# Optimization experiments

Hardware: AMD Instinct MI355X
Metric: run time of the kernel (lower is better)

## Reference

```python
import jax, jax.numpy as jnp
import numpy as np

D_MODEL = 768
N_HEADS = 12
NUM_EXPERTS = 4
TOP_K = 2
SPAN_LEN = 64
GATE_HIDDEN = 128


def setup_inputs() -> dict:
    key = jax.random.key(0)
    ks = jax.random.split(key, 14)
    B, T, C, E = 4, 4096, D_MODEL, NUM_EXPERTS
    s = 0.02
    return {
        "hidden_states": jax.random.normal(ks[0], (B, T, C), jnp.float32),
        "Wq": jax.random.normal(ks[1], (E, C, C), jnp.float32) * s,
        "bq": jnp.zeros((E, C), jnp.float32),
        "Wk": jax.random.normal(ks[2], (E, C, C), jnp.float32) * s,
        "bk": jnp.zeros((E, C), jnp.float32),
        "Wv": jax.random.normal(ks[3], (E, C, C), jnp.float32) * s,
        "bv": jnp.zeros((E, C), jnp.float32),
        "gW1": jax.random.normal(ks[4], (GATE_HIDDEN, C), jnp.float32) * s,
        "gb1": jnp.zeros((GATE_HIDDEN,), jnp.float32),
        "gW2": jax.random.normal(ks[5], (E, GATE_HIDDEN), jnp.float32) * s,
        "gb2": jnp.zeros((E,), jnp.float32),
        "Wo": jax.random.normal(ks[6], (C, C), jnp.float32) * s,
        "bo": jnp.zeros((C,), jnp.float32),
    }


def _moe_proj(w, x, W, b):
    # per-expert projection then gate-weighted sum over experts
    # x: (B,N,S,C), W: (E,O,C), w: (B,N,E)
    proj = jnp.einsum("bnsc,eoc->ebnso", x, W)          # (E,B,N,S,C)
    out = jnp.einsum("bne,ebnso->bnso", w, proj)
    out = out + jnp.einsum("bne,eo->bno", w, b)[:, :, None, :]
    return out


def reference(hidden_states, Wq, bq, Wk, bk, Wv, bv, gW1, gb1, gW2, gb2, Wo, bo):
    B, T, C = hidden_states.shape
    S, H, E, K = SPAN_LEN, N_HEADS, NUM_EXPERTS, TOP_K
    Dh = C // H
    N = T // S  # T is a multiple of span_len -> no padding, all-ones masks
    x = hidden_states.reshape(B, N, S, C)

    # gating: mean-pool per span -> MLP -> top-k softmax scattered to E slots
    pooled = x.mean(axis=2)                                  # (B,N,C)
    h = jax.nn.relu(pooled @ gW1.T + gb1)
    logits = h @ gW2.T + gb2                                 # (B,N,E)
    vals, idx = jax.lax.top_k(logits, K)
    sm = jax.nn.softmax(vals, axis=-1)                       # (B,N,K)
    w = jnp.sum(jax.nn.one_hot(idx, E, dtype=sm.dtype) * sm[..., None], axis=-2)  # (B,N,E)
    entropy = -jnp.mean(jnp.sum(w * jnp.log(jnp.clip(w, 1e-9)), axis=-1))

    # gate-weighted expert QKV projections
    q = _moe_proj(w, x, Wq, bq).reshape(B, N, S, H, Dh)
    k = _moe_proj(w, x, Wk, bk).reshape(B, N, S, H, Dh)
    v = _moe_proj(w, x, Wv, bv).reshape(B, N, S, H, Dh)

    # per-span attention (mask is all ones; dropout in eval mode)
    scores = jnp.einsum("bnshd,bnthd->bnhst", q, k) / jnp.sqrt(jnp.float32(Dh))
    attn = jax.nn.softmax(scores, axis=-1)
    out = jnp.einsum("bnhst,bnthd->bnshd", attn, v).reshape(B, T, C)
    out = out @ Wo.T + bo
    return out, entropy
```

## Files before the change

kernel.cpp:

```cpp
#include <hip/hip_runtime.h>
#include <hip/hip_bf16.h>
#include <hip/hip_fp16.h>

typedef _Float16 f16;
typedef _Float16 f16x8 __attribute__((ext_vector_type(8)));
typedef _Float16 f16x4 __attribute__((ext_vector_type(4)));
typedef float f32x4 __attribute__((ext_vector_type(4)));

constexpr int B = 4;
constexpr int T = 4096;
constexpr int C = 768;
constexpr int NH = 12;
constexpr int DH = 64;
constexpr int E = 4;
constexpr int SPAN = 64;
constexpr int N = T / SPAN;
constexpr int BN = B * N;
constexpr int GH = 128;
constexpr int BTC = B * T * C;

constexpr int U_WO = C * C / 8;

#define LGKM_BARRIER()                                      \
    do {                                                    \
        asm volatile("s_waitcnt lgkmcnt(0)" ::: "memory");  \
        __builtin_amdgcn_s_barrier();                       \
        __builtin_amdgcn_sched_barrier(0);                  \
    } while (0)

__global__ __launch_bounds__(768) void cvt_x_pool(
    const float* __restrict__ x, f16* __restrict__ x16,
    float* __restrict__ pooled) {
    int span = blockIdx.x;
    int tid = threadIdx.x;
    int u = tid % 96, rg = tid / 96;
    __shared__ f16x8 xlds[6144];
    __shared__ float part[8][C];

    const float* xb = x + (size_t)span * SPAN * C;
    float a8[8] = {};
    #pragma unroll
    for (int j = 0; j < 8; ++j) {
        int r = rg * 8 + j;
        const float4* s = (const float4*)(xb + (size_t)r * C + u * 8);
        float4 A = s[0], Bv = s[1];
        f16x8 o;
        o[0] = (f16)A.x;  o[1] = (f16)A.y;  o[2] = (f16)A.z;  o[3] = (f16)A.w;
        o[4] = (f16)Bv.x; o[5] = (f16)Bv.y; o[6] = (f16)Bv.z; o[7] = (f16)Bv.w;
        xlds[r * 96 + (u & ~7) + ((u & 7) ^ (r & 7))] = o;
        a8[0] += A.x;  a8[1] += A.y;  a8[2] += A.z;  a8[3] += A.w;
        a8[4] += Bv.x; a8[5] += Bv.y; a8[6] += Bv.z; a8[7] += Bv.w;
    }
    #pragma unroll
    for (int j = 0; j < 8; ++j) part[rg][u * 8 + j] = a8[j];
    __syncthreads();
    float s = 0.f;
    #pragma unroll
    for (int g = 0; g < 8; ++g) s += part[g][tid];
    pooled[(size_t)span * C + tid] = s * (1.f / 64.f);

    f16x8* xo = (f16x8*)x16 + (size_t)span * 6144;
    #pragma unroll
    for (int j = 0; j < 8; ++j) {
        int un = tid + j * 768;
        int lr = un & 15, lg = (un >> 4) & 3, m = (un >> 6) & 3, kt = un >> 8;
        int row = m * 16 + lr, ku = kt * 4 + lg;
        xo[un] = xlds[row * 96 + (ku & ~7) + ((ku & 7) ^ (row & 7))];
    }
}

__global__ __launch_bounds__(768) void cvt_w_frag(
    const float* __restrict__ Wq, const float* __restrict__ Wk,
    const float* __restrict__ Wv,
    f16* __restrict__ Wq16, f16* __restrict__ Wk16, f16* __restrict__ Wv16) {
    int slice = blockIdx.x;
    int tsel  = blockIdx.y;
    const float* src; f16* dst;
    if (tsel == 0)      { src = Wq; dst = Wq16; }
    else if (tsel == 1) { src = Wk; dst = Wk16; }
    else                { src = Wv; dst = Wv16; }
    int e = slice / 12, cb = slice % 12;

    __shared__ f16x8 wlds[6144];
    int tid = threadIdx.x;

    const float* wb = src + ((size_t)e * C + cb * 64) * C;
    #pragma unroll
    for (int j = 0; j < 8; ++j) {
        int g = tid + j * 768;
        int row = g / 96, ku = g % 96;
        const float4* sp = (const float4*)(wb + (size_t)row * C + ku * 8);
        float4 A = sp[0], Bv = sp[1];
        f16x8 o;
        o[0] = (f16)A.x;  o[1] = (f16)A.y;  o[2] = (f16)A.z;  o[3] = (f16)A.w;
        o[4] = (f16)Bv.x; o[5] = (f16)Bv.y; o[6] = (f16)Bv.z; o[7] = (f16)Bv.w;
        wlds[row * 96 + (ku & ~7) + ((ku & 7) ^ (row & 7))] = o;
    }
    __syncthreads();

    f16x8* wo = (f16x8*)dst + (size_t)slice * 6144;
    #pragma unroll
    for (int j = 0; j < 8; ++j) {
        int un = tid + j * 768;
        int lr = un & 15, lg = (un >> 4) & 3, nn = (un >> 6) & 3, kt = un >> 8;
        int row = nn * 16 + lr, ku = kt * 4 + lg;
        wo[un] = wlds[row * 96 + (ku & ~7) + ((ku & 7) ^ (row & 7))];
    }
}

__global__ void cvt_wo(const float* __restrict__ Wo, f16* __restrict__ Wo16) {
    int i = blockIdx.x * blockDim.x + threadIdx.x;
    int stride = gridDim.x * blockDim.x;
    for (; i < U_WO; i += stride) {
        float4 a = ((const float4*)Wo)[2 * i];
        float4 b = ((const float4*)Wo)[2 * i + 1];
        f16x8 o;
        o[0] = (f16)a.x; o[1] = (f16)a.y; o[2] = (f16)a.z; o[3] = (f16)a.w;
        o[4] = (f16)b.x; o[5] = (f16)b.y; o[6] = (f16)b.z; o[7] = (f16)b.w;
        ((f16x8*)Wo16)[i] = o;
    }
}

__global__ __launch_bounds__(128) void gate_mlp(
    const float* __restrict__ pooled,
    const float* __restrict__ gW1, const float* __restrict__ gb1,
    const float* __restrict__ gW2, const float* __restrict__ gb2,
    int* __restrict__ eidx, float* __restrict__ ewts,
    float* __restrict__ ent_partial) {
    int span = blockIdx.x;
    int tid = threadIdx.x;
    __shared__ float pl[C];
    __shared__ float h[GH];
    __shared__ float logits[E];

    for (int c = tid; c < C; c += 128) pl[c] = pooled[(size_t)span * C + c];
    __syncthreads();

    {
        float acc = gb1[tid];
        const float* wrow = gW1 + (size_t)tid * C;
        #pragma unroll 8
        for (int c = 0; c < C; ++c) acc += pl[c] * wrow[c];
        h[tid] = acc > 0.f ? acc : 0.f;
    }
    __syncthreads();

    if (tid < E) {
        float acc = gb2[tid];
        const float* wrow = gW2 + (size_t)tid * GH;
        #pragma unroll 8
        for (int j = 0; j < GH; ++j) acc += h[j] * wrow[j];
        logits[tid] = acc;
    }
    __syncthreads();

    if (tid == 0) {
        int i0 = 0; float v0 = logits[0];
        for (int e = 1; e < E; ++e) { if (logits[e] > v0) { v0 = logits[e]; i0 = e; } }
        int i1 = -1; float v1 = -3.0e38f;
        for (int e = 0; e < E; ++e) { if (e != i0 && logits[e] > v1) { v1 = logits[e]; i1 = e; } }
        float bq_ = expf(v1 - v0);
        float s = 1.f + bq_;
        float sm0 = 1.f / s;
        float sm1 = bq_ / s;
        eidx[span * 2 + 0] = i0;
        eidx[span * 2 + 1] = i1;
        ewts[span * 2 + 0] = sm0;
        ewts[span * 2 + 1] = sm1;
        float p0 = fmaxf(sm0, 1e-9f), p1 = fmaxf(sm1, 1e-9f);
        ent_partial[span] = sm0 * logf(p0) + sm1 * logf(p1);
    }
}

__global__ void entropy_kernel(const float* __restrict__ ent_partial, float* __restrict__ out_ent) {
    __shared__ float sh[256];
    int tid = threadIdx.x;
    sh[tid] = ent_partial[tid];
    __syncthreads();
    for (int s = 128; s > 0; s >>= 1) {
        if (tid < s) sh[tid] += sh[tid + s];
        __syncthreads();
    }
    if (tid == 0) *out_ent = -sh[0] * (1.0f / (float)BN);
}

__global__ __launch_bounds__(256, 2) void qkv_mfma(
    const f16* __restrict__ xh,
    const f16* __restrict__ Wq16, const float* __restrict__ bq,
    const f16* __restrict__ Wk16, const float* __restrict__ bk,
    const f16* __restrict__ Wv16, const float* __restrict__ bv,
    const int* __restrict__ eidx, const float* __restrict__ ewts,
    f16* __restrict__ q16, f16* __restrict__ k16, f16* __restrict__ vt)
{
    int span  = blockIdx.x;
    int otile = blockIdx.y;
    int proj  = blockIdx.z;

    const f16* W; const float* bias; f16* out;
    if (proj == 0)      { W = Wq16; bias = bq; out = q16; }
    else if (proj == 1) { W = Wk16; bias = bk; out = k16; }
    else                { W = Wv16; bias = bv; out = vt; }

    int e0 = eidx[span * 2 + 0], e1 = eidx[span * 2 + 1];
    float w0 = ewts[span * 2 + 0], w1 = ewts[span * 2 + 1];
    f16 w0h = (f16)w0, w1h = (f16)w1;

    int tid = threadIdx.x;
    int lane = tid & 63, wv = tid >> 6;
    int lr = lane & 15, lg = lane >> 4;
    int cb = otile * 4 + wv;

    const f16x8* xu  = (const f16x8*)xh + (size_t)span * 6144 + lane;
    const f16x8* wu0 = (const f16x8*)W + ((size_t)e0 * 12 + cb) * 6144 + lane;
    const f16x8* wu1 = (const f16x8*)W + ((size_t)e1 * 12 + cb) * 6144 + lane;

    f32x4 acc[4][4] = {};

    f16x8 bb0[3][4], bb1[3][4];
    f16x8 aa[2][4];

    #pragma unroll
    for (int n = 0; n < 4; ++n) { bb0[0][n] = wu0[n * 64];        bb1[0][n] = wu1[n * 64]; }
    #pragma unroll
    for (int n = 0; n < 4; ++n) { bb0[1][n] = wu0[(4 + n) * 64];  bb1[1][n] = wu1[(4 + n) * 64]; }
    #pragma unroll
    for (int m = 0; m < 4; ++m) aa[0][m] = xu[m * 64];

    #pragma unroll
    for (int kt = 0; kt < 24; ++kt) {
        if (kt < 22) {
            int kn = kt + 2, s = (kt + 2) % 3;
            #pragma unroll
            for (int n = 0; n < 4; ++n) {
                bb0[s][n] = wu0[(kn * 4 + n) * 64];
                bb1[s][n] = wu1[(kn * 4 + n) * 64];
            }
        }
        if (kt < 23) {
            int kn = kt + 1, s = (kt + 1) & 1;
            #pragma unroll
            for (int m = 0; m < 4; ++m) aa[s][m] = xu[(kn * 4 + m) * 64];
        }

        {
            int s3 = kt % 3, s2 = kt & 1;
            __builtin_amdgcn_s_setprio(1);
            #pragma unroll
            for (int n = 0; n < 4; ++n) {
                f16x8 bf = bb0[s3][n] * w0h + bb1[s3][n] * w1h;
                #pragma unroll
                for (int m = 0; m < 4; ++m)
                    acc[m][n] = __builtin_amdgcn_mfma_f32_16x16x32_f16(aa[s2][m], bf, acc[m][n], 0, 0, 0);
            }
            __builtin_amdgcn_s_setprio(0);
        }
    }

    if (proj == 2) {
        f16* vtb = out + (size_t)span * C * 64;
        #pragma unroll
        for (int n = 0; n < 4; ++n) {
            int col = cb * 64 + n * 16 + lr;
            float be = w0 * bias[(size_t)e0 * C + col] + w1 * bias[(size_t)e1 * C + col];
            #pragma unroll
            for (int m = 0; m < 4; ++m) {
                f16x4 pk;
                #pragma unroll
                for (int r = 0; r < 4; ++r) pk[r] = (f16)(acc[m][n][r] + be);
                *(f16x4*)&vtb[(size_t)col * 64 + m * 16 + lg * 4] = pk;
            }
        }
    } else {
        f16* outb = out + (size_t)span * 64 * C;
        #pragma unroll
        for (int n = 0; n < 4; ++n) {
            int col = cb * 64 + n * 16 + lr;
            float be = w0 * bias[(size_t)e0 * C + col] + w1 * bias[(size_t)e1 * C + col];
            #pragma unroll
            for (int m = 0; m < 4; ++m) {
                #pragma unroll
                for (int r = 0; r < 4; ++r) {
                    int row = m * 16 + lg * 4 + r;
                    outb[(size_t)row * C + col] = (f16)(acc[m][n][r] + be);
                }
            }
        }
    }
}

__global__ __launch_bounds__(256) void attn_mfma(
    const f16* __restrict__ q16, const f16* __restrict__ k16,
    const f16* __restrict__ vt, f16* __restrict__ a16)
{
    int h = blockIdx.x, span = blockIdx.y;
    __shared__ __align__(16) f16 Klds[64 * 72];
    __shared__ __align__(16) f16 Vlds[64 * 72];
    __shared__ __align__(16) f16 Plds[64 * 72];

    int tid = threadIdx.x;
    int lane = tid & 63, mt = tid >> 6;
    int lr = lane & 15, lg = lane >> 4;

    const f16x8* ku = (const f16x8*)k16;
    const f16x8* vu = (const f16x8*)vt;
    #pragma unroll
    for (int i = 0; i < 2; ++i) {
        int id = tid + i * 256;
        int r = id >> 3, u = id & 7;
        *(f16x8*)&Klds[r * 72 + u * 8] = ku[(size_t)span * 6144 + (size_t)r * 96 + h * 8 + u];
        *(f16x8*)&Vlds[r * 72 + u * 8] = vu[(size_t)span * 6144 + (size_t)(h * 64 + r) * 8 + u];
    }
    const f16x8* qu = (const f16x8*)q16;
    f16x8 qa[2];
    #pragma unroll
    for (int kk = 0; kk < 2; ++kk)
        qa[kk] = qu[(size_t)span * 6144 + (size_t)(mt * 16 + lr) * 96 + h * 8 + kk * 4 + lg];

    LGKM_BARRIER();

    f32x4 accs[4] = {};
    #pragma unroll
    for (int nt = 0; nt < 4; ++nt) {
        #pragma unroll
        for (int kk = 0; kk < 2; ++kk) {
            f16x8 kb = *(const f16x8*)&Klds[(nt * 16 + lr) * 72 + kk * 32 + lg * 8];
            accs[nt] = __builtin_amdgcn_mfma_f32_16x16x32_f16(qa[kk], kb, accs[nt], 0, 0, 0);
        }
    }

    #pragma unroll
    for (int nt = 0; nt < 4; ++nt) accs[nt] *= 0.125f;
    f32x4 m4;
    #pragma unroll
    for (int r = 0; r < 4; ++r)
        m4[r] = fmaxf(fmaxf(accs[0][r], accs[1][r]), fmaxf(accs[2][r], accs[3][r]));
    #pragma unroll
    for (int st = 1; st < 16; st <<= 1) {
        #pragma unroll
        for (int r = 0; r < 4; ++r) m4[r] = fmaxf(m4[r], __shfl_xor(m4[r], st));
    }
    f32x4 ps[4];
    f32x4 sum4 = {0.f, 0.f, 0.f, 0.f};
    #pragma unroll
    for (int nt = 0; nt < 4; ++nt)
        #pragma unroll
        for (int r = 0; r < 4; ++r) {
            ps[nt][r] = __expf(accs[nt][r] - m4[r]);
            sum4[r] += ps[nt][r];
        }
    #pragma unroll
    for (int st = 1; st < 16; st <<= 1) {
        #pragma unroll
        for (int r = 0; r < 4; ++r) sum4[r] += __shfl_xor(sum4[r], st);
    }
    f32x4 inv4;
    #pragma unroll
    for (int r = 0; r < 4; ++r) inv4[r] = 1.0f / sum4[r];

    #pragma unroll
    for (int nt = 0; nt < 4; ++nt)
        #pragma unroll
        for (int r = 0; r < 4; ++r)
            Plds[(mt * 16 + lg * 4 + r) * 72 + nt * 16 + lr] = (f16)ps[nt][r];

    LGKM_BARRIER();

    f16x8 pa[2];
    #pragma unroll
    for (int kkt = 0; kkt < 2; ++kkt)
        pa[kkt] = *(const f16x8*)&Plds[(mt * 16 + lr) * 72 + kkt * 32 + lg * 8];
    f32x4 acco[4] = {};
    #pragma unroll
    for (int nt = 0; nt < 4; ++nt) {
        #pragma unroll
        for (int kkt = 0; kkt < 2; ++kkt) {
            f16x8 vb = *(const f16x8*)&Vlds[(nt * 16 + lr) * 72 + kkt * 32 + lg * 8];
            acco[nt] = __builtin_amdgcn_mfma_f32_16x16x32_f16(pa[kkt], vb, acco[nt], 0, 0, 0);
        }
    }

    #pragma unroll
    for (int nt = 0; nt < 4; ++nt)
        #pragma unroll
        for (int r = 0; r < 4; ++r)
            Klds[(mt * 16 + lg * 4 + r) * 72 + nt * 16 + lr] = (f16)(acco[nt][r] * inv4[r]);

    LGKM_BARRIER();

    int row = mt * 16 + (lane >> 2);
    int u2 = (lane & 3) * 2;
    f16x8 o0 = *(const f16x8*)&Klds[row * 72 + u2 * 8];
    f16x8 o1 = *(const f16x8*)&Klds[row * 72 + u2 * 8 + 8];
    f16x8* au = (f16x8*)a16;
    au[(size_t)span * 6144 + (size_t)row * 96 + h * 8 + u2]     = o0;
    au[(size_t)span * 6144 + (size_t)row * 96 + h * 8 + u2 + 1] = o1;
}

__global__ __launch_bounds__(512) void outproj_mfma(
    const f16* __restrict__ ah, const f16* __restrict__ Wo16,
    const float* __restrict__ bo, float* __restrict__ Y)
{
    int rt = blockIdx.x;
    int otile = blockIdx.y;

    __shared__ f16x8 as_u[128 * 8];
    __shared__ f16x8 ws_u[256 * 8];

    const f16x8* au  = (const f16x8*)(ah + (size_t)rt * 128 * C);
    const f16x8* Wou = (const f16x8*)(Wo16 + (size_t)otile * 256 * C);

    int tid = threadIdx.x;
    int lane = tid & 63, wv = tid >> 6;
    int lr = lane & 15, lg = lane >> 4;
    int wm = (wv >> 2) * 64;
    int wn = (wv & 3) * 64;

    f32x4 acc[4][4] = {};

    f16x8 ar_[2], wr_[4];
    #pragma unroll
    for (int i = 0; i < 2; ++i) {
        int id = tid + i * 512;
        ar_[i] = au[(size_t)(id >> 3) * 96 + (id & 7)];
    }
    #pragma unroll
    for (int i = 0; i < 4; ++i) {
        int id = tid + i * 512;
        wr_[i] = Wou[(size_t)(id >> 3) * 96 + (id & 7)];
    }

    for (int kc8 = 0; kc8 < 96; kc8 += 8) {
        #pragma unroll
        for (int i = 0; i < 2; ++i) {
            int id = tid + i * 512;
            int r = id >> 3, u = id & 7;
            as_u[r * 8 + (u ^ (r & 7))] = ar_[i];
        }
        #pragma unroll
        for (int i = 0; i < 4; ++i) {
            int id = tid + i * 512;
            int r = id >> 3, u = id & 7;
            ws_u[r * 8 + (u ^ (r & 7))] = wr_[i];
        }

        if (kc8 < 88) {
            int kn = kc8 + 8;
            #pragma unroll
            for (int i = 0; i < 2; ++i) {
                int id = tid + i * 512;
                ar_[i] = au[(size_t)(id >> 3) * 96 + kn + (id & 7)];
            }
            #pragma unroll
            for (int i = 0; i < 4; ++i) {
                int id = tid + i * 512;
                wr_[i] = Wou[(size_t)(id >> 3) * 96 + kn + (id & 7)];
            }
        }

        LGKM_BARRIER();

        #pragma unroll
        for (int kk = 0; kk < 2; ++kk) {
            int ub = kk * 4 + lg;
            f16x8 afrag[4], bfrag[4];
            #pragma unroll
            for (int m = 0; m < 4; ++m) {
                int r = wm + m * 16 + lr;
                afrag[m] = as_u[r * 8 + (ub ^ (r & 7))];
            }
            #pragma unroll
            for (int n = 0; n < 4; ++n) {
                int r = wn + n * 16 + lr;
                bfrag[n] = ws_u[r * 8 + (ub ^ (r & 7))];
            }
            #pragma unroll
            for (int m = 0; m < 4; ++m)
                #pragma unroll
                for (int n = 0; n < 4; ++n)
                    acc[m][n] = __builtin_amdgcn_mfma_f32_16x16x32_f16(afrag[m], bfrag[n], acc[m][n], 0, 0, 0);
        }

        LGKM_BARRIER();
    }

    #pragma unroll
    for (int n = 0; n < 4; ++n) {
        int col = otile * 256 + wn + n * 16 + lr;
        float be = bo[col];
        #pragma unroll
        for (int m = 0; m < 4; ++m) {
            #pragma unroll
            for (int r = 0; r < 4; ++r) {
                int row = rt * 128 + wm + m * 16 + lg * 4 + r;
                Y[(size_t)row * C + col] = acc[m][n][r] + be;
            }
        }
    }
}

extern "C" void kernel_launch(void* const* d_in, const int* in_sizes, int n_in,
                              void* d_out, int out_size, void* d_ws, size_t ws_size,
                              hipStream_t stream) {
    const float* x   = (const float*)d_in[0];
    const float* Wq  = (const float*)d_in[1];
    const float* bq  = (const float*)d_in[2];
    const float* Wk  = (const float*)d_in[3];
    const float* bk  = (const float*)d_in[4];
    const float* Wv  = (const float*)d_in[5];
    const float* bv  = (const float*)d_in[6];
    const float* gW1 = (const float*)d_in[7];
    const float* gb1 = (const float*)d_in[8];
    const float* gW2 = (const float*)d_in[9];
    const float* gb2 = (const float*)d_in[10];
    const float* Wo  = (const float*)d_in[11];
    const float* bo  = (const float*)d_in[12];

    float* out = (float*)d_out;

    char* ws = (char*)d_ws;
    const size_t h_btc = (size_t)BTC * sizeof(f16);
    f16* x16  = (f16*)(ws);
    f16* q16  = (f16*)(ws + 1 * h_btc);
    f16* k16  = (f16*)(ws + 2 * h_btc);
    f16* vt16 = (f16*)(ws + 3 * h_btc);
    f16* a16  = (f16*)(ws + 4 * h_btc);
    size_t off = 5 * h_btc;
    const size_t wsz = (size_t)E * C * C * sizeof(f16);
    f16* Wq16 = (f16*)(ws + off); off += wsz;
    f16* Wk16 = (f16*)(ws + off); off += wsz;
    f16* Wv16 = (f16*)(ws + off); off += wsz;
    f16* Wo16 = (f16*)(ws + off); off += (size_t)C * C * sizeof(f16);
    int*   eidx = (int*)(ws + off); off += 2048;
    float* ewts = (float*)(ws + off); off += 2048;
    float* entp = (float*)(ws + off); off += 1024;
    float* pooled = (float*)(ws + off); off += (size_t)BN * C * sizeof(float);

    cvt_x_pool<<<dim3(BN), dim3(768), 0, stream>>>(x, x16, pooled);
    cvt_w_frag<<<dim3(48, 3), dim3(768), 0, stream>>>(Wq, Wk, Wv,
                                                      Wq16, Wk16, Wv16);
    cvt_wo<<<dim3(288), dim3(256), 0, stream>>>(Wo, Wo16);
    gate_mlp<<<dim3(BN), dim3(128), 0, stream>>>(pooled, gW1, gb1, gW2, gb2,
                                                 eidx, ewts, entp);
    entropy_kernel<<<dim3(1), dim3(256), 0, stream>>>(entp, out + BTC);

    qkv_mfma<<<dim3(BN, 3, 3), dim3(256), 0, stream>>>(x16, Wq16, bq, Wk16, bk, Wv16, bv,
                                                       eidx, ewts, q16, k16, vt16);
    attn_mfma<<<dim3(NH, BN), dim3(256), 0, stream>>>(q16, k16, vt16, a16);
    outproj_mfma<<<dim3(128, 3), dim3(512), 0, stream>>>(a16, Wo16, bo, out);
}
```

Baseline: 209.5 us.

## Pair spans sharing the same expert pair to reuse weight loads in QKV GEMM

Adds a small kernel that groups spans by their unordered top-2 expert pair and packs them two per slot. The QKV kernel then processes two spans per block with a halved output-column tile, so each weight fragment loaded from global memory serves both spans. This halves per-span weight traffic. In exchange it adds a serial single-block launch, blocks that exit early when they fall beyond the slot count, and more register pressure from doubled activation buffers.

```diff
diff --git a/kernel.cpp b/kernel.cpp
--- a/kernel.cpp
+++ b/kernel.cpp
@@ -184,15 +184,56 @@
     if (tid == 0) *out_ent = -sh[0] * (1.0f / (float)BN);
 }
 
+constexpr int MAXSLOTS = 131;
+
+__global__ __launch_bounds__(256) void pair_spans(
+    const int* __restrict__ eidx,
+    int* __restrict__ slotA, int* __restrict__ slotB, int* __restrict__ nslots)
+{
+    __shared__ int cnt[16];
+    __shared__ int base[16];
+    __shared__ int pos[16];
+    __shared__ int list[256];
+    int t = threadIdx.x;
+    if (t < 16) cnt[t] = 0;
+    __syncthreads();
+    int a = eidx[t * 2], b = eidx[t * 2 + 1];
+    int lo = a < b ? a : b, hi = a < b ? b : a;
+    int key = lo * 4 + hi;
+    atomicAdd(&cnt[key], 1);
+    __syncthreads();
+    if (t == 0) {
+        int acc = 0;
+        for (int k = 0; k < 16; ++k) { base[k] = acc; pos[k] = acc; acc += cnt[k]; }
+    }
+    __syncthreads();
+    int p = atomicAdd(&pos[key], 1);
+    list[p] = t;
+    __syncthreads();
+    if (t == 0) {
+        int ns = 0;
+        for (int k = 0; k < 16; ++k) {
+            int s = base[k], c = cnt[k];
+            int i = 0;
+            for (; i + 1 < c; i += 2) { slotA[ns] = list[s + i]; slotB[ns] = list[s + i + 1]; ++ns; }
+            if (i < c) { slotA[ns] = list[s + i]; slotB[ns] = -1; ++ns; }
+        }
+        *nslots = ns;
+    }
+}
+
 __global__ __launch_bounds__(256, 2) void qkv_mfma(
     const f16* __restrict__ xh,
     const f16* __restrict__ Wq16, const float* __restrict__ bq,
     const f16* __restrict__ Wk16, const float* __restrict__ bk,
     const f16* __restrict__ Wv16, const float* __restrict__ bv,
     const int* __restrict__ eidx, const float* __restrict__ ewts,
+    const int* __restrict__ slotA, const int* __restrict__ slotB,
+    const int* __restrict__ nslots,
     f16* __restrict__ q16, f16* __restrict__ k16, f16* __restrict__ vt)
 {
-    int span  = blockIdx.x;
+    int slot = blockIdx.x;
+    if (slot >= *nslots) return;
     int otile = blockIdx.y;
     int proj  = blockIdx.z;
 
@@ -201,87 +242,117 @@
     else if (proj == 1) { W = Wk16; bias = bk; out = k16; }
     else                { W = Wv16; bias = bv; out = vt; }
 
-    int e0 = eidx[span * 2 + 0], e1 = eidx[span * 2 + 1];
-    float w0 = ewts[span * 2 + 0], w1 = ewts[span * 2 + 1];
-    f16 w0h = (f16)w0, w1h = (f16)w1;
+    int spA = slotA[slot];
+    int spBr = slotB[slot];
+    bool isPair = spBr >= 0;
+    int spB = isPair ? spBr : spA;
+
+    int a0 = eidx[spA * 2], a1 = eidx[spA * 2 + 1];
+    int ea = a0 < a1 ? a0 : a1, eb = a0 < a1 ? a1 : a0;
+    float wA0 = ewts[spA * 2], wA1 = ewts[spA * 2 + 1];
+    float wAa = (a0 == ea) ? wA0 : wA1;
+    float wAb = (a0 == ea) ? wA1 : wA0;
+    int b0s = eidx[spB * 2];
+    float wB0 = ewts[spB * 2], wB1 = ewts[spB * 2 + 1];
+    float wBa = (b0s == ea) ? wB0 : wB1;
+    float wBb = (b0s == ea) ? wB1 : wB0;
+    f16 wAah = (f16)wAa, wAbh = (f16)wAb, wBah = (f16)wBa, wBbh = (f16)wBb;
 
     int tid = threadIdx.x;
     int lane = tid & 63, wv = tid >> 6;
     int lr = lane & 15, lg = lane >> 4;
-    int cb = otile * 4 + wv;
-
-    const f16x8* xu  = (const f16x8*)xh + (size_t)span * 6144 + lane;
-    const f16x8* wu0 = (const f16x8*)W + ((size_t)e0 * 12 + cb) * 6144 + lane;
-    const f16x8* wu1 = (const f16x8*)W + ((size_t)e1 * 12 + cb) * 6144 + lane;
-
-    f32x4 acc[4][4] = {};
-
-    f16x8 bb0[3][4], bb1[3][4];
-    f16x8 aa[2][4];
-
-    #pragma unroll
-    for (int n = 0; n < 4; ++n) { bb0[0][n] = wu0[n * 64];        bb1[0][n] = wu1[n * 64]; }
-    #pragma unroll
-    for (int n = 0; n < 4; ++n) { bb0[1][n] = wu0[(4 + n) * 64];  bb1[1][n] = wu1[(4 + n) * 64]; }
-    #pragma unroll
-    for (int m = 0; m < 4; ++m) aa[0][m] = xu[m * 64];
+    int co = otile * 4 + wv;
+    int cb = co >> 1;
+    int nh = (co & 1) * 2;
+
+    const f16x8* xuA = (const f16x8*)xh + (size_t)spA * 6144 + lane;
+    const f16x8* xuB = (const f16x8*)xh + (size_t)spB * 6144 + lane;
+    const f16x8* wua = (const f16x8*)W + ((size_t)ea * 12 + cb) * 6144 + nh * 64 + lane;
+    const f16x8* wub = (const f16x8*)W + ((size_t)eb * 12 + cb) * 6144 + nh * 64 + lane;
+
+    f32x4 acc[2][4][2] = {};
+
+    f16x8 aa[2][2][4];
+    f16x8 ba[3][2], bb[3][2];
+
+    #pragma unroll
+    for (int n = 0; n < 2; ++n) { ba[0][n] = wua[n * 64];        bb[0][n] = wub[n * 64]; }
+    #pragma unroll
+    for (int n = 0; n < 2; ++n) { ba[1][n] = wua[(4 + n) * 64];  bb[1][n] = wub[(4 + n) * 64]; }
+    #pragma unroll
+    for (int m = 0; m < 4; ++m) { aa[0][0][m] = xuA[m * 64];     aa[0][1][m] = xuB[m * 64]; }
 
     #pragma unroll
     for (int kt = 0; kt < 24; ++kt) {
         if (kt < 22) {
             int kn = kt + 2, s = (kt + 2) % 3;
             #pragma unroll
-            for (int n = 0; n < 4; ++n) {
-                bb0[s][n] = wu0[(kn * 4 + n) * 64];
-                bb1[s][n] = wu1[(kn * 4 + n) * 64];
+            for (int n = 0; n < 2; ++n) {
+                ba[s][n] = wua[(kn * 4 + n) * 64];
+                bb[s][n] = wub[(kn * 4 + n) * 64];
             }
         }
         if (kt < 23) {
             int kn = kt + 1, s = (kt + 1) & 1;
             #pragma unroll
-            for (int m = 0; m < 4; ++m) aa[s][m] = xu[(kn * 4 + m) * 64];
+            for (int m = 0; m < 4; ++m) {
+                aa[s][0][m] = xuA[(kn * 4 + m) * 64];
+                aa[s][1][m] = xuB[(kn * 4 + m) * 64];
+            }
         }
 
         {
             int s3 = kt % 3, s2 = kt & 1;
             __builtin_amdgcn_s_setprio(1);
             #pragma unroll
-            for (int n = 0; n < 4; ++n) {
-                f16x8 bf = bb0[s3][n] * w0h + bb1[s3][n] * w1h;
+            for (int n = 0; n < 2; ++n) {
+                f16x8 bfA = ba[s3][n] * wAah + bb[s3][n] * wAbh;
+                f16x8 bfB = ba[s3][n] * wBah + bb[s3][n] * wBbh;
                 #pragma unroll
                 for (int m = 0; m < 4; ++m)
-                    acc[m][n] = __builtin_amdgcn_mfma_f32_16x16x32_f16(aa[s2][m], bf, acc[m][n], 0, 0, 0);
+                    acc[0][m][n] = __builtin_amdgcn_mfma_f32_16x16x32_f16(aa[s2][0][m], bfA, acc[0][m][n], 0, 0, 0);
+                #pragma unroll
+                for (int m = 0; m < 4; ++m)
+                    acc[1][m][n] = __builtin_amdgcn_mfma_f32_16x16x32_f16(aa[s2][1][m], bfB, acc[1][m][n], 0, 0, 0);
             }
             __builtin_amdgcn_s_setprio(0);
         }
     }
 
-    if (proj == 2) {
-        f16* vtb = out + (size_t)span * C * 64;
-        #pragma unroll
-        for (int n = 0; n < 4; ++n) {
-            int col = cb * 64 + n * 16 + lr;
-            float be = w0 * bias[(size_t)e0 * C + col] + w1 * bias[(size_t)e1 * C + col];
-            #pragma unroll
-            for (int m = 0; m < 4; ++m) {
-                f16x4 pk;
+    #pragma unroll
+    for (int sp = 0; sp < 2; ++sp) {
+        if (sp == 1 && !isPair) break;
+        int span = sp ? spB : spA;
+        float wa = sp ? wBa : wAa;
+        float wb2 = sp ? wBb : wAb;
+
+        if (proj == 2) {
+            f16* vtb = out + (size_t)span * C * 64;
+            #pragma unroll
+            for (int n = 0; n < 2; ++n) {
+                int col = co * 32 + n * 16 + lr;
+                float be = wa * bias[(size_t)ea * C + col] + wb2 * bias[(size_t)eb * C + col];
                 #pragma unroll
-                for (int r = 0; r < 4; ++r) pk[r] = (f16)(acc[m][n][r] + be);
-                *(f16x4*)&vtb[(size_t)col * 64 + m * 16 + lg * 4] = pk;
-            }
-        }
-    } else {
-        f16* outb = out + (size_t)span * 64 * C;
-        #pragma unroll
-        for (int n = 0; n < 4; ++n) {
-            int col = cb * 64 + n * 16 + lr;
-            float be = w0 * bias[(size_t)e0 * C + col] + w1 * bias[(size_t)e1 * C + col];
-            #pragma unroll
-            for (int m = 0; m < 4; ++m) {
+                for (int m = 0; m < 4; ++m) {
+                    f16x4 pk;
+                    #pragma unroll
+                    for (int r = 0; r < 4; ++r) pk[r] = (f16)(acc[sp][m][n][r] + be);
+                    *(f16x4*)&vtb[(size_t)col * 64 + m * 16 + lg * 4] = pk;
+                }
+            }
+        } else {
+            f16* outb = out + (size_t)span * 64 * C;
+            #pragma unroll
+            for (int n = 0; n < 2; ++n) {
+                int col = co * 32 + n * 16 + lr;
+                float be = wa * bias[(size_t)ea * C + col] + wb2 * bias[(size_t)eb * C + col];
                 #pragma unroll
-                for (int r = 0; r < 4; ++r) {
-                    int row = m * 16 + lg * 4 + r;
-                    outb[(size_t)row * C + col] = (f16)(acc[m][n][r] + be);
+                for (int m = 0; m < 4; ++m) {
+                    #pragma unroll
+                    for (int r = 0; r < 4; ++r) {
+                        int row = m * 16 + lg * 4 + r;
+                        outb[(size_t)row * C + col] = (f16)(acc[sp][m][n][r] + be);
+                    }
                 }
             }
         }
@@ -534,6 +605,9 @@
     float* ewts = (float*)(ws + off); off += 2048;
     float* entp = (float*)(ws + off); off += 1024;
     float* pooled = (float*)(ws + off); off += (size_t)BN * C * sizeof(float);
+    int* slotA  = (int*)(ws + off); off += 1024;
+    int* slotB  = (int*)(ws + off); off += 1024;
+    int* nslots = (int*)(ws + off); off += 256;
 
     cvt_x_pool<<<dim3(BN), dim3(768), 0, stream>>>(x, x16, pooled);
     cvt_w_frag<<<dim3(48, 3), dim3(768), 0, stream>>>(Wq, Wk, Wv,
@@ -541,10 +615,12 @@
     cvt_wo<<<dim3(288), dim3(256), 0, stream>>>(Wo, Wo16);
     gate_mlp<<<dim3(BN), dim3(128), 0, stream>>>(pooled, gW1, gb1, gW2, gb2,
                                                  eidx, ewts, entp);
+    pair_spans<<<dim3(1), dim3(256), 0, stream>>>(eidx, slotA, slotB, nslots);
     entropy_kernel<<<dim3(1), dim3(256), 0, stream>>>(entp, out + BTC);
 
-    qkv_mfma<<<dim3(BN, 3, 3), dim3(256), 0, stream>>>(x16, Wq16, bq, Wk16, bk, Wv16, bv,
-                                                       eidx, ewts, q16, k16, vt16);
+    qkv_mfma<<<dim3(MAXSLOTS, 6, 3), dim3(256), 0, stream>>>(
+        x16, Wq16, bq, Wk16, bk, Wv16, bv,
+        eidx, ewts, slotA, slotB, nslots, q16, k16, vt16);
     attn_mfma<<<dim3(NH, BN), dim3(256), 0, stream>>>(q16, k16, vt16, a16);
     outproj_mfma<<<dim3(128, 3), dim3(512), 0, stream>>>(a16, Wo16, bo, out);
 }
```

Measured after the change: 234.3 us. +11.8%, slower.
